# Optimization experiments

Measured on AMD Instinct MI355X. Metric: run time of the kernel, lower is better.

## Reference

```python
import jax, jax.numpy as jnp
import numpy as np

B, S, H, I, E = 4, 2048, 768, 3072, 8
TOP_K = 2
ALPHA_BALANCE = 0.01
ENERGY_ALPHA = 0.0


def setup_inputs() -> dict:
    key = jax.random.key(0)
    ks = jax.random.split(key, 5)
    g = lambda k, shape: jax.random.normal(k, shape, jnp.float32) * 0.02
    return {
        "hidden_states": jax.random.normal(ks[0], (B, S, H), jnp.float32),
        "router_w": g(ks[1], (H, E)),
        "router_b": jnp.zeros((E,), jnp.float32),
        "w1": g(ks[2], (E, H, I)),
        "b1": jnp.zeros((E, I), jnp.float32),
        "w2": g(ks[3], (E, I, H)),
        "b2": jnp.zeros((E, H), jnp.float32),
    }


def reference(hidden_states, router_w, router_b, w1, b1, w2, b2):
    # --- routing: top-2 softmax gate scattered back to dense [B,S,E] ---
    router_logits = hidden_states @ router_w + router_b          # [B,S,E]
    top_v, top_i = jax.lax.top_k(router_logits, TOP_K)           # [B,S,2]
    top_w = jax.nn.softmax(top_v, axis=-1)                       # [B,S,2]
    gating = jnp.sum(
        jax.nn.one_hot(top_i, E, dtype=router_logits.dtype) * top_w[..., None],
        axis=-2,
    )                                                            # [B,S,E]

    # --- aux losses (torch .std() is unbiased, ddof=1) ---
    importance = gating.sum(axis=(0, 1))                         # [E]
    mean_imp = importance.mean()
    load_balancing_loss = ALPHA_BALANCE * (
        jnp.var(importance, ddof=1) / (mean_imp ** 2 + 1e-8)
    )
    probs_mean = gating.mean(axis=(0, 1))                        # [E]
    energy_loss = ENERGY_ALPHA * jnp.sum(probs_mean ** 2)
    aux_loss = load_balancing_loss + energy_loss

    # --- dense all-expert FFN (faithful to the naive original) ---
    # h: [B,S,E,I]; exact (erf) GELU matches torch nn.GELU default
    h = jax.nn.gelu(
        jnp.einsum("bsh,ehf->bsef", hidden_states, w1) + b1,
        approximate=False,
    )
    expert_outputs = jnp.einsum("bsef,efh->bseh", h, w2) + b2    # [B,S,E,H]
    # dropout is identity in eval mode

    # --- weighted combine (the bmm in the original) ---
    final_output = jnp.einsum("bse,bseh->bsh", gating, expert_outputs)
    return final_output, aux_loss, gating
```

## Files before the change

### kernel.cpp

```cpp
#include <hip/hip_runtime.h>
#include <math.h>

#define NB 4
#define NS 2048
#define HD 768
#define ID 3072
#define NE 8
#define NTOK (NB*NS)
#define NPAIR (NTOK*2)

#define BMF 128
#define BNF 256
#define BKF 64
#define MAXTF 136

#define BMS 32
#define KCH 128
#define NCHUNK (ID/KCH)
#define MAXTS (NPAIR/BMS + NE)
#define LDP 36

typedef unsigned short u16;
typedef __attribute__((ext_vector_type(8))) short bf16x8;
typedef __attribute__((ext_vector_type(4))) float f32x4;

__device__ __forceinline__ float bf2f(u16 u) {
  union { unsigned int i; float f; } v; v.i = ((unsigned int)u) << 16; return v.f;
}
__device__ __forceinline__ u16 f2bf(float f) {
  union { float fl; unsigned int i; } v; v.fl = f;
  unsigned int r = v.i + 0x7fffu + ((v.i >> 16) & 1u);
  return (u16)(r >> 16);
}
__device__ __forceinline__ void gload16(const void* g, void* l) {
  __builtin_amdgcn_global_load_lds(
      (const __attribute__((address_space(1))) void*)g,
      (__attribute__((address_space(3))) void*)l, 16, 0, 0);
}
__device__ __forceinline__ float gelu_fast(float x) {
  float u = 0.7978845608028654f * (x + 0.044715f * x * x * x);
  float e = __expf(2.f * u);
  float t = 1.f - 2.f / (e + 1.f);
  return 0.5f * x * (1.f + t);
}

__global__ __launch_bounds__(256) void router_kernel(
    const float* __restrict__ x, const float* __restrict__ rw,
    const float* __restrict__ rb, float* __restrict__ gating,
    int* __restrict__ topi, float* __restrict__ topw)
{
  int wid = threadIdx.x >> 6, lane = threadIdx.x & 63;
  int tok = blockIdx.x * 4 + wid;
  float acc[NE];
  #pragma unroll
  for (int e = 0; e < NE; ++e) acc[e] = 0.f;
  const float* xr = x + (size_t)tok * HD;
  #pragma unroll 4
  for (int r = 0; r < HD/64; ++r) {
    int h = r*64 + lane;
    float xv = xr[h];
    const float4* wr = (const float4*)(rw + (size_t)h*NE);
    float4 a = wr[0], b = wr[1];
    acc[0] += xv*a.x; acc[1] += xv*a.y; acc[2] += xv*a.z; acc[3] += xv*a.w;
    acc[4] += xv*b.x; acc[5] += xv*b.y; acc[6] += xv*b.z; acc[7] += xv*b.w;
  }
  #pragma unroll
  for (int off = 1; off < 64; off <<= 1) {
    #pragma unroll
    for (int e = 0; e < NE; ++e) acc[e] += __shfl_xor(acc[e], off);
  }
  float lg[NE];
  #pragma unroll
  for (int e = 0; e < NE; ++e) lg[e] = acc[e] + rb[e];
  int i0 = 0;
  #pragma unroll
  for (int e = 1; e < NE; ++e) if (lg[e] > lg[i0]) i0 = e;
  int i1 = (i0 == 0) ? 1 : 0;
  #pragma unroll
  for (int e = 0; e < NE; ++e) if (e != i0 && lg[e] > lg[i1]) i1 = e;
  float ex = expf(lg[i1] - lg[i0]);
  float s = 1.f + ex;
  float w0 = 1.f / s, w1v = ex / s;
  if (lane < NE)
    gating[(size_t)tok*NE + lane] = (lane==i0) ? w0 : (lane==i1 ? w1v : 0.f);
  if (lane == 0) {
    topi[2*tok] = i0; topi[2*tok+1] = i1;
    topw[2*tok] = w0; topw[2*tok+1] = w1v;
  }
}

__global__ __launch_bounds__(1024) void plan_kernel(
    const int* __restrict__ topi, const float* __restrict__ topw,
    int* __restrict__ offs, int* __restrict__ tilesc,
    int* __restrict__ ptok, float* __restrict__ pwv, int bm,
    float* __restrict__ aux)
{
  __shared__ int   wcnt[16][NE];
  __shared__ int   wbase[16][NE];
  __shared__ float wsum[16][NE];
  int tid = threadIdx.x, w = tid >> 6, lane = tid & 63;
  int base = w * 1024;

  int cnt[NE];
  #pragma unroll
  for (int e = 0; e < NE; ++e) cnt[e] = 0;
  #pragma unroll
  for (int it = 0; it < 16; ++it) {
    int ti = topi[base + it*64 + lane];
    #pragma unroll
    for (int e = 0; e < NE; ++e) {
      unsigned long long m = __ballot(ti == e);
      cnt[e] += __popcll(m);
    }
  }
  if (lane == 0)
    #pragma unroll
    for (int e = 0; e < NE; ++e) wcnt[w][e] = cnt[e];
  __syncthreads();

  if (tid == 0) {
    int o = 0, tt = 0;
    for (int e = 0; e < NE; ++e) {
      offs[e] = o; tilesc[e] = tt;
      int run = o, tot = 0;
      for (int ww = 0; ww < 16; ++ww) { wbase[ww][e] = run; run += wcnt[ww][e]; tot += wcnt[ww][e]; }
      o += tot;
      tt += (tot + bm - 1) / bm;
    }
    offs[NE] = o; tilesc[NE] = tt;
  }
  __syncthreads();

  int run[NE];
  float lsum[NE];
  #pragma unroll
  for (int e = 0; e < NE; ++e) { run[e] = wbase[w][e]; lsum[e] = 0.f; }
  unsigned long long lt = (1ull << lane) - 1ull;
  #pragma unroll
  for (int it = 0; it < 16; ++it) {
    int p = base + it*64 + lane;
    int ti = topi[p];
    float tw = topw[p];
    int idx = 0;
    #pragma unroll
    for (int e = 0; e < NE; ++e) {
      unsigned long long m = __ballot(ti == e);
      int r = run[e] + __popcll(m & lt);
      if (ti == e) idx = r;
      run[e] += __popcll(m);
      lsum[e] += (ti == e) ? tw : 0.f;
    }
    ptok[idx] = p >> 1;
    pwv[idx] = tw;
  }
  #pragma unroll
  for (int off = 1; off < 64; off <<= 1) {
    #pragma unroll
    for (int e = 0; e < NE; ++e) lsum[e] += __shfl_xor(lsum[e], off);
  }
  if (lane == 0)
    #pragma unroll
    for (int e = 0; e < NE; ++e) wsum[w][e] = lsum[e];
  __syncthreads();
  if (tid == 0) {
    float imp[NE];
    for (int e = 0; e < NE; ++e) {
      float s = 0.f;
      for (int ww = 0; ww < 16; ++ww) s += wsum[ww][e];
      imp[e] = s;
    }
    float mean = 0.f;
    for (int e = 0; e < NE; ++e) mean += imp[e];
    mean *= (1.f/NE);
    float var = 0.f;
    for (int e = 0; e < NE; ++e) { float d = imp[e] - mean; var += d*d; }
    var *= (1.f/(NE-1));
    aux[0] = 0.01f * var / (mean*mean + 1e-8f);
  }
}

__global__ __launch_bounds__(256) void cvt_x_kernel(
    const float* __restrict__ x, u16* __restrict__ xb)
{
  int i = (blockIdx.x * 256 + threadIdx.x) * 8;
  float4 a = *(const float4*)&x[i];
  float4 b = *(const float4*)&x[i + 4];
  uint4 o;
  o.x = (unsigned)f2bf(a.x) | ((unsigned)f2bf(a.y) << 16);
  o.y = (unsigned)f2bf(a.z) | ((unsigned)f2bf(a.w) << 16);
  o.z = (unsigned)f2bf(b.x) | ((unsigned)f2bf(b.y) << 16);
  o.w = (unsigned)f2bf(b.z) | ((unsigned)f2bf(b.w) << 16);
  *(uint4*)&xb[i] = o;
}

__global__ __launch_bounds__(256) void transpose_bf16_kernel(
    const float* __restrict__ src, u16* __restrict__ dst, int R, int C)
{
  __shared__ u16 tile[64][65];
  int e = blockIdx.z;
  const float* s = src + (size_t)e * R * C;
  u16* d = dst + (size_t)e * R * C;
  int c0 = blockIdx.x * 64, r0 = blockIdx.y * 64;
  int t = threadIdx.x;
  int rr = t >> 4, c4 = (t & 15) * 4;
  #pragma unroll
  for (int rep = 0; rep < 4; ++rep) {
    int r = rr + rep * 16;
    float4 v = *(const float4*)&s[(size_t)(r0 + r) * C + c0 + c4];
    tile[r][c4+0] = f2bf(v.x); tile[r][c4+1] = f2bf(v.y);
    tile[r][c4+2] = f2bf(v.z); tile[r][c4+3] = f2bf(v.w);
  }
  __syncthreads();
  #pragma unroll
  for (int rep = 0; rep < 4; ++rep) {
    int w = t + rep * 256;
    int c = w >> 4, rq = (w & 15) * 4;
    ushort4 o;
    o.x = tile[rq+0][c]; o.y = tile[rq+1][c];
    o.z = tile[rq+2][c]; o.w = tile[rq+3][c];
    *(ushort4*)&d[(size_t)(c0 + c) * R + r0 + rq] = o;
  }
}

__global__ __launch_bounds__(512, 2) void moe_gemm1_kernel(
    const u16* __restrict__ xbf, const u16* __restrict__ w1t,
    const float* __restrict__ b1, const int* __restrict__ offs,
    const int* __restrict__ tilesc, const int* __restrict__ ptok,
    const float* __restrict__ pwv, u16* __restrict__ hbuf, int t0)
{
  __shared__ __align__(16) u16 As[BMF*BKF];
  __shared__ __align__(16) u16 Bs[BNF*BKF];
  __shared__ int   toks_s[BMF];
  __shared__ float gws_s[BMF];

  int t = t0 + blockIdx.x;
  if (t >= tilesc[NE]) return;
  int e = 0;
  #pragma unroll
  for (int k = 1; k < NE; ++k) if (t >= tilesc[k]) e = k;
  int row0 = offs[e] + (t - tilesc[e]) * BMF;
  int nrows = offs[e+1] - row0; if (nrows > BMF) nrows = BMF;
  int n0 = blockIdx.y * BNF;
  int tid = threadIdx.x, wid = tid >> 6, lane = tid & 63;

  if (tid < BMF) {
    int tk = -1; float g = 0.f;
    if (tid < nrows) { tk = ptok[row0 + tid]; g = pwv[row0 + tid]; }
    toks_s[tid] = tk; gws_s[tid] = g;
  }
  __syncthreads();

  int ssub = tid >> 3;
  int sbc  = (tid & 7) << 4;
  int swz  = sbc ^ ((ssub & 7) << 4);
  int tkA0 = toks_s[ssub];      if (tkA0 < 0) tkA0 = 0;
  int tkA1 = toks_s[64 + ssub]; if (tkA1 < 0) tkA1 = 0;
  const char* aS0 = (const char*)xbf + (size_t)tkA0 * (HD*2) + swz;
  const char* aS1 = (const char*)xbf + (size_t)tkA1 * (HD*2) + swz;
  const char* bS0 = (const char*)w1t + ((size_t)e*ID + n0 +       ssub) * (HD*2) + swz;
  const char* bS1 = (const char*)w1t + ((size_t)e*ID + n0 +  64 + ssub) * (HD*2) + swz;
  const char* bS2 = (const char*)w1t + ((size_t)e*ID + n0 + 128 + ssub) * (HD*2) + swz;
  const char* bS3 = (const char*)w1t + ((size_t)e*ID + n0 + 192 + ssub) * (HD*2) + swz;
  u16* aD0 = As + wid*512;
  u16* aD1 = As + 4096 + wid*512;
  u16* bD0 = Bs + wid*512;
  u16* bD1 = Bs +  4096 + wid*512;
  u16* bD2 = Bs +  8192 + wid*512;
  u16* bD3 = Bs + 12288 + wid*512;

  int wr = wid >> 2, wc = wid & 3;
  int lr = lane & 15, lg = lane >> 4;

  f32x4 acc[4][4];
  #pragma unroll
  for (int m = 0; m < 4; ++m)
    #pragma unroll
    for (int n = 0; n < 4; ++n) { f32x4 z = {0.f,0.f,0.f,0.f}; acc[m][n] = z; }

  for (int ks = 0; ks < HD/BKF; ++ks) {
    __syncthreads();
    int ko = ks * 128;
    gload16(aS0 + ko, aD0);
    gload16(aS1 + ko, aD1);
    gload16(bS0 + ko, bD0);
    gload16(bS1 + ko, bD1);
    gload16(bS2 + ko, bD2);
    gload16(bS3 + ko, bD3);
    __syncthreads();
    #pragma unroll
    for (int k2 = 0; k2 < 2; ++k2) {
      bf16x8 af[4], bfr[4];
      #pragma unroll
      for (int m = 0; m < 4; ++m) {
        int row = wr*64 + m*16 + lr;
        int bo = (k2*64 + lg*16) ^ ((row & 7) << 4);
        af[m] = *(const bf16x8*)((const char*)As + row*128 + bo);
      }
      #pragma unroll
      for (int n = 0; n < 4; ++n) {
        int row = wc*64 + n*16 + lr;
        int bo = (k2*64 + lg*16) ^ ((row & 7) << 4);
        bfr[n] = *(const bf16x8*)((const char*)Bs + row*128 + bo);
      }
      #pragma unroll
      for (int m = 0; m < 4; ++m)
        #pragma unroll
        for (int n = 0; n < 4; ++n)
          acc[m][n] = __builtin_amdgcn_mfma_f32_16x16x32_bf16(af[m], bfr[n], acc[m][n], 0, 0, 0);
    }
  }

  int rbase = wr*64, cbase = n0 + wc*64;
  const float* b1e = b1 + (size_t)e * ID;
  float b1v[4];
  #pragma unroll
  for (int n = 0; n < 4; ++n) b1v[n] = b1e[cbase + n*16 + lr];
  size_t hrow0 = (size_t)blockIdx.x * BMF;
  #pragma unroll
  for (int m = 0; m < 4; ++m) {
    #pragma unroll
    for (int j = 0; j < 4; ++j) {
      int row = rbase + m*16 + lg*4 + j;
      float g = gws_s[row];
      u16* hp = hbuf + (hrow0 + row) * ID + cbase + lr;
      #pragma unroll
      for (int n = 0; n < 4; ++n) {
        float v = acc[m][n][j] + b1v[n];
        hp[n*16] = f2bf(gelu_fast(v) * g);
      }
    }
  }
}

__global__ __launch_bounds__(512, 2) void moe_gemm2_kernel(
    const u16* __restrict__ hbuf, const u16* __restrict__ w2t,
    const float* __restrict__ b2, const int* __restrict__ offs,
    const int* __restrict__ tilesc, const int* __restrict__ ptok,
    const float* __restrict__ pwv, float* __restrict__ out, int t0)
{
  __shared__ __align__(16) u16 As[BMF*BKF];
  __shared__ __align__(16) u16 Bs[BNF*BKF];
  __shared__ int   toks_s[BMF];
  __shared__ float gws_s[BMF];

  int t = t0 + blockIdx.x;
  if (t >= tilesc[NE]) return;
  int e = 0;
  #pragma unroll
  for (int k = 1; k < NE; ++k) if (t >= tilesc[k]) e = k;
  int row0 = offs[e] + (t - tilesc[e]) * BMF;
  int nrows = offs[e+1] - row0; if (nrows > BMF) nrows = BMF;
  int n0 = blockIdx.y * BNF;
  int tid = threadIdx.x, wid = tid >> 6, lane = tid & 63;

  if (tid < BMF) {
    int tk = -1; float g = 0.f;
    if (tid < nrows) { tk = ptok[row0 + tid]; g = pwv[row0 + tid]; }
    toks_s[tid] = tk; gws_s[tid] = g;
  }
  __syncthreads();

  int ssub = tid >> 3;
  int sbc  = (tid & 7) << 4;
  int swz  = sbc ^ ((ssub & 7) << 4);
  const char* aS0 = (const char*)hbuf + ((size_t)blockIdx.x*BMF +       ssub) * (ID*2) + swz;
  const char* aS1 = (const char*)hbuf + ((size_t)blockIdx.x*BMF +  64 + ssub) * (ID*2) + swz;
  const char* bS0 = (const char*)w2t + ((size_t)e*HD + n0 +       ssub) * (ID*2) + swz;
  const char* bS1 = (const char*)w2t + ((size_t)e*HD + n0 +  64 + ssub) * (ID*2) + swz;
  const char* bS2 = (const char*)w2t + ((size_t)e*HD + n0 + 128 + ssub) * (ID*2) + swz;
  const char* bS3 = (const char*)w2t + ((size_t)e*HD + n0 + 192 + ssub) * (ID*2) + swz;
  u16* aD0 = As + wid*512;
  u16* aD1 = As + 4096 + wid*512;
  u16* bD0 = Bs + wid*512;
  u16* bD1 = Bs +  4096 + wid*512;
  u16* bD2 = Bs +  8192 + wid*512;
  u16* bD3 = Bs + 12288 + wid*512;

  int wr = wid >> 2, wc = wid & 3;
  int lr = lane & 15, lg = lane >> 4;

  f32x4 acc[4][4];
  #pragma unroll
  for (int m = 0; m < 4; ++m)
    #pragma unroll
    for (int n = 0; n < 4; ++n) { f32x4 z = {0.f,0.f,0.f,0.f}; acc[m][n] = z; }

  for (int ks = 0; ks < ID/BKF; ++ks) {
    __syncthreads();
    int ko = ks * 128;
    gload16(aS0 + ko, aD0);
    gload16(aS1 + ko, aD1);
    gload16(bS0 + ko, bD0);
    gload16(bS1 + ko, bD1);
    gload16(bS2 + ko, bD2);
    gload16(bS3 + ko, bD3);
    __syncthreads();
    #pragma unroll
    for (int k2 = 0; k2 < 2; ++k2) {
      bf16x8 af[4], bfr[4];
      #pragma unroll
      for (int m = 0; m < 4; ++m) {
        int row = wr*64 + m*16 + lr;
        int bo = (k2*64 + lg*16) ^ ((row & 7) << 4);
        af[m] = *(const bf16x8*)((const char*)As + row*128 + bo);
      }
      #pragma unroll
      for (int n = 0; n < 4; ++n) {
        int row = wc*64 + n*16 + lr;
        int bo = (k2*64 + lg*16) ^ ((row & 7) << 4);
        bfr[n] = *(const bf16x8*)((const char*)Bs + row*128 + bo);
      }
      #pragma unroll
      for (int m = 0; m < 4; ++m)
        #pragma unroll
        for (int n = 0; n < 4; ++n)
          acc[m][n] = __builtin_amdgcn_mfma_f32_16x16x32_bf16(af[m], bfr[n], acc[m][n], 0, 0, 0);
    }
  }

  int rbase = wr*64, cbase = n0 + wc*64;
  const float* b2e = b2 + (size_t)e * HD;
  float b2v[4];
  #pragma unroll
  for (int n = 0; n < 4; ++n) b2v[n] = b2e[cbase + n*16 + lr];
  #pragma unroll
  for (int m = 0; m < 4; ++m) {
    #pragma unroll
    for (int j = 0; j < 4; ++j) {
      int row = rbase + m*16 + lg*4 + j;
      int tk = toks_s[row];
      if (tk < 0) continue;
      float g = gws_s[row];
      float* op = out + (size_t)tk * HD + cbase + lr;
      #pragma unroll
      for (int n = 0; n < 4; ++n)
        atomicAdd(&op[n*16], acc[m][n][j] + g * b2v[n]);
    }
  }
}

__global__ __launch_bounds__(512, 4) void ffn_kernel(
    const float* __restrict__ x, const float* __restrict__ w1,
    const float* __restrict__ b1, const float* __restrict__ w2,
    const float* __restrict__ b2, const int* __restrict__ offs,
    const int* __restrict__ tilesc, const int* __restrict__ ptok,
    const float* __restrict__ pwv, float* __restrict__ out)
{
  __shared__ u16 x_t[HD][LDP];
  __shared__ u16 h_t[KCH][LDP];
  __shared__ int   toks[BMS];
  __shared__ float gws[BMS];

  int bid = blockIdx.x;
  if (bid >= tilesc[NE]) return;
  int e = 0;
  #pragma unroll
  for (int k = 1; k < NE; ++k) if (bid >= tilesc[k]) e = k;
  int tile = bid - tilesc[e];
  int row0 = offs[e] + tile * BMS;
  int nrows = offs[e+1] - row0;
  if (nrows > BMS) nrows = BMS;

  int tid = threadIdx.x;
  if (tid < BMS) {
    int tk = -1; float g = 0.f;
    if (tid < nrows) { tk = ptok[row0 + tid]; g = pwv[row0 + tid]; }
    toks[tid] = tk; gws[tid] = g;
  }
  __syncthreads();

  for (int idx = tid; idx < BMS*HD; idx += 512) {
    int m = idx / HD, h = idx - m*HD;
    int tk = toks[m];
    x_t[h][m] = (tk >= 0) ? f2bf(x[(size_t)tk*HD + h]) : (u16)0;
  }

  int w4 = (tid >> 6) << 2;
  int lane = tid & 63;
  const float* w1e = w1 + (size_t)e * HD * ID;
  const float* w2e = w2 + (size_t)e * ID * HD;
  const float* b1e = b1 + (size_t)e * ID;
  const float* b2e = b2 + (size_t)e * HD;

  float acc[4][12];
  #pragma unroll
  for (int jm = 0; jm < 4; ++jm)
    #pragma unroll
    for (int jn = 0; jn < 12; ++jn) acc[jm][jn] = 0.f;

  __syncthreads();
  float gwr[4];
  #pragma unroll
  for (int jm = 0; jm < 4; ++jm) gwr[jm] = gws[w4 + jm];

  for (int c = 0; c < NCHUNK; ++c) {
    int i0 = c * KCH;
    float hb[4][2];
    #pragma unroll
    for (int jm = 0; jm < 4; ++jm) { hb[jm][0] = 0.f; hb[jm][1] = 0.f; }
    const float* p = w1e + i0 + lane;
    #pragma unroll 4
    for (int h = 0; h < HD; ++h) {
      ushort4 xu = *(const ushort4*)&x_t[h][w4];
      float wv0 = p[0];
      float wv1 = p[64];
      p += ID;
      float x0 = bf2f(xu.x), x1 = bf2f(xu.y), x2 = bf2f(xu.z), x3 = bf2f(xu.w);
      hb[0][0] += x0*wv0; hb[1][0] += x1*wv0; hb[2][0] += x2*wv0; hb[3][0] += x3*wv0;
      hb[0][1] += x0*wv1; hb[1][1] += x1*wv1; hb[2][1] += x2*wv1; hb[3][1] += x3*wv1;
    }
    float b1v0 = b1e[i0 + lane];
    float b1v1 = b1e[i0 + 64 + lane];
    __syncthreads();
    #pragma unroll
    for (int q = 0; q < 2; ++q) {
      int il = lane + 64*q;
      float bv = q ? b1v1 : b1v0;
      #pragma unroll
      for (int jm = 0; jm < 4; ++jm) {
        float v = hb[jm][q] + bv;
        v = 0.5f * v * (1.f + erff(v * 0.70710678118654752f));
        h_t[il][w4 + jm] = f2bf(v * gwr[jm]);
      }
    }
    __syncthreads();
    const float* q2 = w2e + (size_t)i0 * HD + lane;
    for (int k = 0; k < KCH; ++k) {
      ushort4 hu = *(const ushort4*)&h_t[k][w4];
      float h0 = bf2f(hu.x), h1 = bf2f(hu.y), h2 = bf2f(hu.z), h3 = bf2f(hu.w);
      #pragma unroll
      for (int jn = 0; jn < 12; ++jn) {
        float wv = q2[64*jn];
        acc[0][jn] += h0*wv; acc[1][jn] += h1*wv;
        acc[2][jn] += h2*wv; acc[3][jn] += h3*wv;
      }
      q2 += HD;
    }
  }

  #pragma unroll
  for (int jm = 0; jm < 4; ++jm) {
    int m = w4 + jm;
    int tk = toks[m];
    if (tk < 0) continue;
    float g = gwr[jm];
    float* orow = out + (size_t)tk * HD;
    #pragma unroll
    for (int jn = 0; jn < 12; ++jn) {
      int n = lane + 64*jn;
      atomicAdd(&orow[n], acc[jm][jn] + g * b2e[n]);
    }
  }
}

extern "C" void kernel_launch(void* const* d_in, const int* in_sizes, int n_in,
                              void* d_out, int out_size, void* d_ws, size_t ws_size,
                              hipStream_t stream)
{
  const float* x  = (const float*)d_in[0];
  const float* rw = (const float*)d_in[1];
  const float* rb = (const float*)d_in[2];
  const float* w1 = (const float*)d_in[3];
  const float* b1 = (const float*)d_in[4];
  const float* w2 = (const float*)d_in[5];
  const float* b2 = (const float*)d_in[6];

  float* out    = (float*)d_out;
  float* aux    = out + (size_t)NTOK * HD;
  float* gating = aux + 1;

  int*   W  = (int*)d_ws;
  float* Wf = (float*)d_ws;
  int*   offs   = W + 16;
  int*   tilesc = W + 32;
  int*   topi   = W + 64;
  float* topw   = Wf + 64 + NPAIR;
  int*   ptok   = W + 64 + 2*NPAIR;
  float* pwv    = Wf + 64 + 3*NPAIR;
  char*  wsB    = (char*)d_ws;
  const size_t OFF_XBF = 262400;
  const size_t OFF_W1T = OFF_XBF + (size_t)NTOK*HD*2;
  const size_t OFF_W2T = OFF_W1T + (size_t)NE*ID*HD*2;
  const size_t OFF_H   = OFF_W2T + (size_t)NE*ID*HD*2;
  const size_t NEED_FULL = OFF_H + (size_t)MAXTF*BMF*ID*2;
  const size_t NEED_2    = OFF_H + (size_t)68*BMF*ID*2;

  u16* xbf = (u16*)(wsB + OFF_XBF);
  u16* w1t = (u16*)(wsB + OFF_W1T);
  u16* w2t = (u16*)(wsB + OFF_W2T);
  u16* hb  = (u16*)(wsB + OFF_H);

  hipMemsetAsync(d_out, 0, (size_t)NTOK * HD * sizeof(float), stream);

  router_kernel<<<NTOK/4, 256, 0, stream>>>(x, rw, rb, gating, topi, topw);

  if (ws_size >= NEED_2) {
    plan_kernel<<<1, 1024, 0, stream>>>(topi, topw, offs, tilesc, ptok, pwv, BMF, aux);
    cvt_x_kernel<<<(NTOK*HD)/(8*256), 256, 0, stream>>>(x, xbf);
    transpose_bf16_kernel<<<dim3(ID/64, HD/64, NE), 256, 0, stream>>>(w1, w1t, HD, ID);
    transpose_bf16_kernel<<<dim3(HD/64, ID/64, NE), 256, 0, stream>>>(w2, w2t, ID, HD);
    int cht = (ws_size >= NEED_FULL) ? MAXTF : 68;
    int nch = (ws_size >= NEED_FULL) ? 1 : 2;
    for (int c = 0; c < nch; ++c) {
      moe_gemm1_kernel<<<dim3(cht, ID/BNF), 512, 0, stream>>>(
          xbf, w1t, b1, offs, tilesc, ptok, pwv, hb, c*cht);
      moe_gemm2_kernel<<<dim3(cht, HD/BNF), 512, 0, stream>>>(
          hb, w2t, b2, offs, tilesc, ptok, pwv, out, c*cht);
    }
  } else {
    plan_kernel<<<1, 1024, 0, stream>>>(topi, topw, offs, tilesc, ptok, pwv, BMS, aux);
    ffn_kernel<<<MAXTS, 512, 0, stream>>>(x, w1, b1, w2, b2, offs, tilesc, ptok, pwv, out);
  }
}
```

Measured before the change: 318.2 us.

## Split-K GEMM2 over two slices, XCD-aware block swizzle, vectorize router loads

GEMM2 is split along K into two halves via gridDim.z, and each half accumulates with atomics into the output. Only the first slice adds the bias. Both grouped GEMMs remap block IDs so that neighbouring tiles land on the same XCD, which should improve L2 reuse of expert weights. The router loop now uses float4 loads of x. This doubles the atomic traffic in GEMM2 in exchange for more parallelism, since its grid was small (136x3 blocks).

```diff
diff --git a/kernel.cpp b/kernel.cpp
--- a/kernel.cpp
+++ b/kernel.cpp
@@ -13,6 +13,7 @@
 #define BNF 256
 #define BKF 64
 #define MAXTF 136
+#define KS2 24
 
 #define BMS 32
 #define KCH 128
@@ -43,6 +44,13 @@
   float t = 1.f - 2.f / (e + 1.f);
   return 0.5f * x * (1.f + t);
 }
+__device__ __forceinline__ int xcd_swz_2d() {
+  int nwg  = gridDim.x * gridDim.y;
+  int orig = blockIdx.x + blockIdx.y * gridDim.x;
+  int q = nwg >> 3, r = nwg & 7;
+  int xcd = orig & 7, i = orig >> 3;
+  return (xcd < r) ? (xcd * (q + 1) + i) : (r * (q + 1) + (xcd - r) * q + i);
+}
 
 __global__ __launch_bounds__(256) void router_kernel(
     const float* __restrict__ x, const float* __restrict__ rw,
@@ -55,14 +63,21 @@
   #pragma unroll
   for (int e = 0; e < NE; ++e) acc[e] = 0.f;
   const float* xr = x + (size_t)tok * HD;
-  #pragma unroll 4
-  for (int r = 0; r < HD/64; ++r) {
-    int h = r*64 + lane;
-    float xv = xr[h];
-    const float4* wr = (const float4*)(rw + (size_t)h*NE);
-    float4 a = wr[0], b = wr[1];
-    acc[0] += xv*a.x; acc[1] += xv*a.y; acc[2] += xv*a.z; acc[3] += xv*a.w;
-    acc[4] += xv*b.x; acc[5] += xv*b.y; acc[6] += xv*b.z; acc[7] += xv*b.w;
+  #pragma unroll
+  for (int r = 0; r < 3; ++r) {
+    int h4 = (r*64 + lane) * 4;
+    float4 xv = *(const float4*)&xr[h4];
+    const float4* wr = (const float4*)(rw + (size_t)h4 * NE);
+    float4 a0 = wr[0], c0 = wr[1], a1 = wr[2], c1 = wr[3];
+    float4 a2 = wr[4], c2 = wr[5], a3 = wr[6], c3 = wr[7];
+    acc[0] += xv.x*a0.x + xv.y*a1.x + xv.z*a2.x + xv.w*a3.x;
+    acc[1] += xv.x*a0.y + xv.y*a1.y + xv.z*a2.y + xv.w*a3.y;
+    acc[2] += xv.x*a0.z + xv.y*a1.z + xv.z*a2.z + xv.w*a3.z;
+    acc[3] += xv.x*a0.w + xv.y*a1.w + xv.z*a2.w + xv.w*a3.w;
+    acc[4] += xv.x*c0.x + xv.y*c1.x + xv.z*c2.x + xv.w*c3.x;
+    acc[5] += xv.x*c0.y + xv.y*c1.y + xv.z*c2.y + xv.w*c3.y;
+    acc[6] += xv.x*c0.z + xv.y*c1.z + xv.z*c2.z + xv.w*c3.z;
+    acc[7] += xv.x*c0.w + xv.y*c1.w + xv.z*c2.w + xv.w*c3.w;
   }
   #pragma unroll
   for (int off = 1; off < 64; off <<= 1) {
@@ -233,14 +248,17 @@
   __shared__ int   toks_s[BMF];
   __shared__ float gws_s[BMF];
 
-  int t = t0 + blockIdx.x;
+  int wkid = xcd_swz_2d();
+  int tile = wkid % gridDim.x;
+  int n0   = (wkid / gridDim.x) * BNF;
+
+  int t = t0 + tile;
   if (t >= tilesc[NE]) return;
   int e = 0;
   #pragma unroll
   for (int k = 1; k < NE; ++k) if (t >= tilesc[k]) e = k;
   int row0 = offs[e] + (t - tilesc[e]) * BMF;
   int nrows = offs[e+1] - row0; if (nrows > BMF) nrows = BMF;
-  int n0 = blockIdx.y * BNF;
   int tid = threadIdx.x, wid = tid >> 6, lane = tid & 63;
 
   if (tid < BMF) {
@@ -315,7 +333,7 @@
   float b1v[4];
   #pragma unroll
   for (int n = 0; n < 4; ++n) b1v[n] = b1e[cbase + n*16 + lr];
-  size_t hrow0 = (size_t)blockIdx.x * BMF;
+  size_t hrow0 = (size_t)tile * BMF;
   #pragma unroll
   for (int m = 0; m < 4; ++m) {
     #pragma unroll
@@ -343,14 +361,19 @@
   __shared__ int   toks_s[BMF];
   __shared__ float gws_s[BMF];
 
-  int t = t0 + blockIdx.x;
+  int wkid = xcd_swz_2d();
+  int tile = wkid % gridDim.x;
+  int n0   = (wkid / gridDim.x) * BNF;
+  int z    = blockIdx.z;
+  int kbase = z * KS2 * 128;
+
+  int t = t0 + tile;
   if (t >= tilesc[NE]) return;
   int e = 0;
   #pragma unroll
   for (int k = 1; k < NE; ++k) if (t >= tilesc[k]) e = k;
   int row0 = offs[e] + (t - tilesc[e]) * BMF;
   int nrows = offs[e+1] - row0; if (nrows > BMF) nrows = BMF;
-  int n0 = blockIdx.y * BNF;
   int tid = threadIdx.x, wid = tid >> 6, lane = tid & 63;
 
   if (tid < BMF) {
@@ -363,12 +386,12 @@
   int ssub = tid >> 3;
   int sbc  = (tid & 7) << 4;
   int swz  = sbc ^ ((ssub & 7) << 4);
-  const char* aS0 = (const char*)hbuf + ((size_t)blockIdx.x*BMF +       ssub) * (ID*2) + swz;
-  const char* aS1 = (const char*)hbuf + ((size_t)blockIdx.x*BMF +  64 + ssub) * (ID*2) + swz;
-  const char* bS0 = (const char*)w2t + ((size_t)e*HD + n0 +       ssub) * (ID*2) + swz;
-  const char* bS1 = (const char*)w2t + ((size_t)e*HD + n0 +  64 + ssub) * (ID*2) + swz;
-  const char* bS2 = (const char*)w2t + ((size_t)e*HD + n0 + 128 + ssub) * (ID*2) + swz;
-  const char* bS3 = (const char*)w2t + ((size_t)e*HD + n0 + 192 + ssub) * (ID*2) + swz;
+  const char* aS0 = (const char*)hbuf + ((size_t)tile*BMF +       ssub) * (ID*2) + swz + kbase;
+  const char* aS1 = (const char*)hbuf + ((size_t)tile*BMF +  64 + ssub) * (ID*2) + swz + kbase;
+  const char* bS0 = (const char*)w2t + ((size_t)e*HD + n0 +       ssub) * (ID*2) + swz + kbase;
+  const char* bS1 = (const char*)w2t + ((size_t)e*HD + n0 +  64 + ssub) * (ID*2) + swz + kbase;
+  const char* bS2 = (const char*)w2t + ((size_t)e*HD + n0 + 128 + ssub) * (ID*2) + swz + kbase;
+  const char* bS3 = (const char*)w2t + ((size_t)e*HD + n0 + 192 + ssub) * (ID*2) + swz + kbase;
   u16* aD0 = As + wid*512;
   u16* aD1 = As + 4096 + wid*512;
   u16* bD0 = Bs + wid*512;
@@ -383,9 +406,9 @@
   #pragma unroll
   for (int m = 0; m < 4; ++m)
     #pragma unroll
-    for (int n = 0; n < 4; ++n) { f32x4 z = {0.f,0.f,0.f,0.f}; acc[m][n] = z; }
-
-  for (int ks = 0; ks < ID/BKF; ++ks) {
+    for (int n = 0; n < 4; ++n) { f32x4 zz = {0.f,0.f,0.f,0.f}; acc[m][n] = zz; }
+
+  for (int ks = 0; ks < KS2; ++ks) {
     __syncthreads();
     int ko = ks * 128;
     gload16(aS0 + ko, aD0);
@@ -422,7 +445,7 @@
   const float* b2e = b2 + (size_t)e * HD;
   float b2v[4];
   #pragma unroll
-  for (int n = 0; n < 4; ++n) b2v[n] = b2e[cbase + n*16 + lr];
+  for (int n = 0; n < 4; ++n) b2v[n] = (z == 0) ? b2e[cbase + n*16 + lr] : 0.f;
   #pragma unroll
   for (int m = 0; m < 4; ++m) {
     #pragma unroll
@@ -604,7 +627,7 @@
     for (int c = 0; c < nch; ++c) {
       moe_gemm1_kernel<<<dim3(cht, ID/BNF), 512, 0, stream>>>(
           xbf, w1t, b1, offs, tilesc, ptok, pwv, hb, c*cht);
-      moe_gemm2_kernel<<<dim3(cht, HD/BNF), 512, 0, stream>>>(
+      moe_gemm2_kernel<<<dim3(cht, HD/BNF, 2), 512, 0, stream>>>(
           hb, w2t, b2, offs, tilesc, ptok, pwv, out, c*cht);
     }
   } else {
```

After: 368.0 us. 15.6% more time.
